# Kernel tuning notes

Measured on AMD Instinct MI355X. Metric: run time of the kernel, lower is better.

## Reference

```python
import jax, jax.numpy as jnp
import numpy as np

H, DK = 16, 64
D = H * DK  # d_model = 1024
B, S = 2, 2048


def setup_inputs() -> dict:
    key = jax.random.key(0)
    ks = jax.random.split(key, 11)
    std = 1.0 / np.sqrt(D)
    inp = {
        "query": jax.random.normal(ks[0], (B, S, D), dtype=jnp.float32),
        "key": jax.random.normal(ks[1], (B, S, D), dtype=jnp.float32),
        "value": jax.random.normal(ks[2], (B, S, D), dtype=jnp.float32),
        "Wq": jax.random.normal(ks[3], (D, D), dtype=jnp.float32) * std,
        "bq": jnp.zeros((D,), dtype=jnp.float32),
        "Wk": jax.random.normal(ks[4], (D, D), dtype=jnp.float32) * std,
        "bk": jnp.zeros((D,), dtype=jnp.float32),
        "Wv": jax.random.normal(ks[5], (D, D), dtype=jnp.float32) * std,
        "bv": jnp.zeros((D,), dtype=jnp.float32),
        "Wo": jax.random.normal(ks[6], (D, D), dtype=jnp.float32) * std,
        "bo": jnp.zeros((D,), dtype=jnp.float32),
    }
    return inp


def reference(query, key, value, Wq, bq, Wk, bk, Wv, bv, Wo, bo):
    # torch.nn.Linear convention: y = x @ W.T + b
    def split_heads(x):
        b, s, _ = x.shape
        return x.reshape(b, s, H, DK).transpose(0, 2, 1, 3)  # [B,H,S,DK]

    q = split_heads(query @ Wq.T + bq)
    k = split_heads(key @ Wk.T + bk)
    v = split_heads(value @ Wv.T + bv)

    scale = 1.0 / jnp.sqrt(jnp.asarray(DK, dtype=q.dtype))
    scores = jnp.einsum("bhqd,bhkd->bhqk", q, k) * scale  # [B,H,S,S]
    p_attn = jax.nn.softmax(scores, axis=-1)
    ctx = jnp.einsum("bhqk,bhkd->bhqd", p_attn, v)  # [B,H,S,DK]

    ctx = ctx.transpose(0, 2, 1, 3).reshape(query.shape[0], -1, H * DK)
    return ctx @ Wo.T + bo
```

## Files before the change

kernel.cpp:

```cpp
#include <hip/hip_runtime.h>
#include <stdint.h>

#define BATCH 2
#define SEQ   2048
#define NHEAD 16
#define DK    64
#define DMODEL 1024
#define MROWS (BATCH*SEQ)

typedef __attribute__((ext_vector_type(8))) __bf16 bf16x8;
typedef __attribute__((ext_vector_type(4))) float f32x4;
typedef __attribute__((ext_vector_type(8))) unsigned short u16x8;
typedef __attribute__((ext_vector_type(4))) unsigned short u16x4;

#define QSCALE 0.18033688f

__device__ __forceinline__ unsigned short f2bf(float f) {
  union { float f; uint32_t u; } c; c.f = f;
  uint32_t u = c.u;
  return (unsigned short)((u + 0x7fffu + ((u >> 16) & 1u)) >> 16);
}

__device__ __forceinline__ void gld16(const void* g, void* lds) {
  __builtin_amdgcn_global_load_lds(
      (const __attribute__((address_space(1))) void*)g,
      (__attribute__((address_space(3))) void*)lds,
      16, 0, 0);
}

__global__ __launch_bounds__(256)
void cvt_all(const float* __restrict__ q, const float* __restrict__ k, const float* __restrict__ v,
             const float* __restrict__ Wq, const float* __restrict__ Wk,
             const float* __restrict__ Wv, const float* __restrict__ Wo,
             unsigned short* __restrict__ Xq, unsigned short* __restrict__ Xk,
             unsigned short* __restrict__ Xv,
             unsigned short* __restrict__ Wqb, unsigned short* __restrict__ Wkb,
             unsigned short* __restrict__ Wvb, unsigned short* __restrict__ Wob) {
  int blk = blockIdx.x;
  const float* in; unsigned short* out; int base;
  if (blk < 6144) {
    int ti = blk >> 11;
    in  = (ti == 0) ? q  : (ti == 1) ? k  : v;
    out = (ti == 0) ? Xq : (ti == 1) ? Xk : Xv;
    base = (blk & 2047) * 2048;
  } else {
    int ti = (blk - 6144) >> 9;
    in  = (ti == 0) ? Wq  : (ti == 1) ? Wk  : (ti == 2) ? Wv  : Wo;
    out = (ti == 0) ? Wqb : (ti == 1) ? Wkb : (ti == 2) ? Wvb : Wob;
    base = ((blk - 6144) & 511) * 2048;
  }
  int i = base + threadIdx.x * 8;
  float4 a = *(const float4*)(in + i);
  float4 b = *(const float4*)(in + i + 4);
  u16x8 o;
  o[0]=f2bf(a.x); o[1]=f2bf(a.y); o[2]=f2bf(a.z); o[3]=f2bf(a.w);
  o[4]=f2bf(b.x); o[5]=f2bf(b.y); o[6]=f2bf(b.z); o[7]=f2bf(b.w);
  *(u16x8*)(out + i) = o;
}

template <int MODE>
__device__ __forceinline__ void gemm_body(unsigned short* __restrict__ lA,
                                          unsigned short* __restrict__ lB,
                                          const unsigned short* __restrict__ X,
                                          const unsigned short* __restrict__ W,
                                          const float* __restrict__ bias,
                                          unsigned short* __restrict__ Yb,
                                          float* __restrict__ Yf,
                                          int rowBase, int colBase) {
  const int t = threadIdx.x;
  const int lane = t & 63, wave = t >> 6;
  const int cl = lane & 15, qd = lane >> 4;
  const int wm = wave >> 1, wn = wave & 1;
  const int srow = t >> 3, sslot = t & 7;

  int aoff[2][4], boff[2][4];
  #pragma unroll
  for (int ks = 0; ks < 2; ks++)
    #pragma unroll
    for (int i = 0; i < 4; i++) {
      int ra = wm * 64 + i * 16 + cl;
      aoff[ks][i] = ra * 64 + ((ks * 4 + qd) ^ (ra & 7)) * 8;
      int rb = wn * 64 + i * 16 + cl;
      boff[ks][i] = rb * 64 + ((ks * 4 + qd) ^ (rb & 7)) * 8;
    }
  const unsigned short* xp[4];
  const unsigned short* wp[4];
  #pragma unroll
  for (int i = 0; i < 4; i++) {
    int r = i * 32 + srow;
    int chunk = sslot ^ (r & 7);
    xp[i] = X + (size_t)(rowBase + r) * DMODEL + chunk * 8;
    wp[i] = W + (size_t)(colBase + r) * DMODEL + chunk * 8;
  }

  f32x4 zero = {0.f, 0.f, 0.f, 0.f};
  f32x4 acc[4][4];
  for (int mt = 0; mt < 4; mt++) for (int nt = 0; nt < 4; nt++) acc[mt][nt] = zero;

  for (int k0 = 0; k0 < DMODEL; k0 += 64) {
    __syncthreads();
    #pragma unroll
    for (int i = 0; i < 4; i++) {
      gld16(xp[i], (char*)lA + i * 4096 + wave * 1024);
      gld16(wp[i], (char*)lB + i * 4096 + wave * 1024);
      xp[i] += 64; wp[i] += 64;
    }
    __syncthreads();
    #pragma unroll
    for (int ks = 0; ks < 2; ks++) {
      bf16x8 af[4], bfr[4];
      #pragma unroll
      for (int mt = 0; mt < 4; mt++) af[mt] = *(const bf16x8*)&lA[aoff[ks][mt]];
      #pragma unroll
      for (int nt = 0; nt < 4; nt++) bfr[nt] = *(const bf16x8*)&lB[boff[ks][nt]];
      #pragma unroll
      for (int mt = 0; mt < 4; mt++)
        #pragma unroll
        for (int nt = 0; nt < 4; nt++) {
          if (MODE == 2)
            acc[mt][nt] = __builtin_amdgcn_mfma_f32_16x16x32_bf16(af[mt], bfr[nt], acc[mt][nt], 0, 0, 0);
          else
            acc[mt][nt] = __builtin_amdgcn_mfma_f32_16x16x32_bf16(bfr[nt], af[mt], acc[mt][nt], 0, 0, 0);
        }
    }
  }

  if (MODE == 2) {
    #pragma unroll
    for (int mt = 0; mt < 4; mt++) {
      int row0 = rowBase + wm * 64 + mt * 16 + qd * 4;
      int bb = row0 >> 11;
      int s_in = row0 & 2047;
      int blk = s_in & ~63;
      int n4 = (s_in & 63) >> 2;
      int l4 = n4 & 7;
      int pos = 8 * (n4 >> 3) + ((l4 < 4) ? 2 * l4 : 2 * (l4 - 4) + 1);
      #pragma unroll
      for (int nt = 0; nt < 4; nt++) {
        int c = colBase + wn * 64 + nt * 16 + cl;
        float bv = bias[c];
        int hh = c >> 6, d = c & 63;
        u16x4 v;
        #pragma unroll
        for (int r = 0; r < 4; r++) v[r] = f2bf(acc[mt][nt][r] + bv);
        *(u16x4*)&Yb[(size_t)((bb * NHEAD + hh) * 64 + d) * SEQ + blk + pos * 4] = v;
      }
    }
  } else {
    #pragma unroll
    for (int nt = 0; nt < 4; nt++) {
      int col = colBase + wn * 64 + nt * 16 + qd * 4;
      f32x4 bv4 = *(const f32x4*)&bias[col];
      #pragma unroll
      for (int mt = 0; mt < 4; mt++) {
        int row = rowBase + wm * 64 + mt * 16 + cl;
        if (MODE == 3) {
          f32x4 v;
          #pragma unroll
          for (int r = 0; r < 4; r++) v[r] = acc[mt][nt][r] + bv4[r];
          *(f32x4*)&Yf[(size_t)row * DMODEL + col] = v;
        } else {
          u16x4 v;
          #pragma unroll
          for (int r = 0; r < 4; r++) {
            float x = acc[mt][nt][r] + bv4[r];
            v[r] = f2bf(MODE == 1 ? x * QSCALE : x);
          }
          *(u16x4*)&Yb[(size_t)row * DMODEL + col] = v;
        }
      }
    }
  }
}

__global__ __launch_bounds__(256)
void gemm_qkv(const unsigned short* __restrict__ Xq, const unsigned short* __restrict__ Xk,
              const unsigned short* __restrict__ Xv,
              const unsigned short* __restrict__ Wq, const unsigned short* __restrict__ Wk,
              const unsigned short* __restrict__ Wv,
              const float* __restrict__ bq, const float* __restrict__ bk,
              const float* __restrict__ bv,
              unsigned short* __restrict__ Q, unsigned short* __restrict__ K,
              unsigned short* __restrict__ VT) {
  __shared__ unsigned short lA[128 * 64];
  __shared__ unsigned short lB[128 * 64];
  int id = blockIdx.x;
  int by = id & 31, bx = id >> 5;
  int z = blockIdx.z;
  if (z == 0)      gemm_body<1>(lA, lB, Xq, Wq, bq, Q,  nullptr, by * 128, bx * 128);
  else if (z == 1) gemm_body<0>(lA, lB, Xk, Wk, bk, K,  nullptr, by * 128, bx * 128);
  else             gemm_body<2>(lA, lB, Xv, Wv, bv, VT, nullptr, by * 128, bx * 128);
}

__global__ __launch_bounds__(256)
void gemm_out(const unsigned short* __restrict__ CTX, const unsigned short* __restrict__ Wo,
              const float* __restrict__ bo, float* __restrict__ out) {
  __shared__ unsigned short lA[128 * 64];
  __shared__ unsigned short lB[128 * 64];
  int id = blockIdx.x;
  int by = id & 31, bx = id >> 5;
  gemm_body<3>(lA, lB, CTX, Wo, bo, nullptr, out, by * 128, bx * 128);
}

__global__ __launch_bounds__(256)
void attn(const unsigned short* __restrict__ Q, const unsigned short* __restrict__ K,
          const unsigned short* __restrict__ VT, unsigned short* __restrict__ CTX) {
  __shared__ unsigned short lK[2 * 64 * 64];
  __shared__ unsigned short lV[2 * 64 * 64];
  const int t = threadIdx.x, lane = t & 63, wave = t >> 6;
  const int cl = lane & 15, qd = lane >> 4;
  const int flat = blockIdx.x + 16 * blockIdx.y + 256 * blockIdx.z;
  const int loc = flat >> 3;
  const int p = (flat & 7) * 4 + (loc >> 4);
  const int qt = loc & 15, h = p & 15, b = p >> 4;
  const int srow = t >> 3, sslot = t & 7;

  #pragma unroll
  for (int half = 0; half < 2; half++)
    #pragma unroll
    for (int i = 0; i < 2; i++) {
      int r = i * 32 + srow;
      int chunk = sslot ^ (r & 7);
      gld16(Q + (size_t)(b * SEQ + qt * 128 + half * 64 + r) * DMODEL + h * 64 + chunk * 8,
            (char*)lK + half * 8192 + i * 4096 + wave * 1024);
    }
  __syncthreads();
  bf16x8 qf[2][2];
  #pragma unroll
  for (int qg = 0; qg < 2; qg++)
    #pragma unroll
    for (int ks = 0; ks < 2; ks++) {
      int r = wave * 16 + cl;
      int slot = (ks * 4 + qd) ^ (r & 7);
      qf[qg][ks] = *(const bf16x8*)&lK[qg * 4096 + r * 64 + slot * 8];
    }
  __syncthreads();

  int ka[8], va[8];
  #pragma unroll
  for (int ks = 0; ks < 2; ks++)
    #pragma unroll
    for (int nt = 0; nt < 4; nt++) {
      int rk = nt * 16 + cl;
      ka[ks * 4 + nt] = rk * 64 + ((ks * 4 + qd) ^ (rk & 7)) * 8;
    }
  #pragma unroll
  for (int ntp = 0; ntp < 2; ntp++)
    #pragma unroll
    for (int dt = 0; dt < 4; dt++) {
      int d = dt * 16 + cl;
      va[ntp * 4 + dt] = d * 64 + ((4 * ntp + qd) ^ (d & 7)) * 8;
    }

  const unsigned short* kp[2];
  const unsigned short* vp[2];
  #pragma unroll
  for (int i = 0; i < 2; i++) {
    int r = i * 32 + srow;
    int chunk = sslot ^ (r & 7);
    kp[i] = K + (size_t)(b * SEQ + r) * DMODEL + h * 64 + chunk * 8;
    vp[i] = VT + (size_t)((b * NHEAD + h) * 64 + r) * SEQ + chunk * 8;
    gld16(kp[i], (char*)lK + i * 4096 + wave * 1024);
    gld16(vp[i], (char*)lV + i * 4096 + wave * 1024);
    kp[i] += 64 * DMODEL; vp[i] += 64;
  }

  f32x4 zero = {0.f, 0.f, 0.f, 0.f};
  f32x4 o[2][4];
  f32x4 osum[2];
  #pragma unroll
  for (int qg = 0; qg < 2; qg++) {
    #pragma unroll
    for (int dt = 0; dt < 4; dt++) o[qg][dt] = zero;
    osum[qg] = zero;
  }
  bf16x8 ones;
  #pragma unroll
  for (int j = 0; j < 8; j++) ones[j] = (__bf16)1.0f;

  #pragma unroll 2
  for (int kt = 0; kt < SEQ / 64; kt++) {
    const int cb = (kt & 1) * 4096;
    __syncthreads();
    if (kt + 1 < SEQ / 64) {
      const int nb = ((kt + 1) & 1) * 8192;
      #pragma unroll
      for (int i = 0; i < 2; i++) {
        gld16(kp[i], (char*)lK + nb + i * 4096 + wave * 1024);
        gld16(vp[i], (char*)lV + nb + i * 4096 + wave * 1024);
        kp[i] += 64 * DMODEL; vp[i] += 64;
      }
    }

    f32x4 sc[2][4];
    #pragma unroll
    for (int qg = 0; qg < 2; qg++)
      #pragma unroll
      for (int nt = 0; nt < 4; nt++) sc[qg][nt] = zero;
    #pragma unroll
    for (int ks = 0; ks < 2; ks++)
      #pragma unroll
      for (int nt = 0; nt < 4; nt++) {
        bf16x8 kf = *(const bf16x8*)&lK[cb + ka[ks * 4 + nt]];
        sc[0][nt] = __builtin_amdgcn_mfma_f32_16x16x32_bf16(kf, qf[0][ks], sc[0][nt], 0, 0, 0);
        sc[1][nt] = __builtin_amdgcn_mfma_f32_16x16x32_bf16(kf, qf[1][ks], sc[1][nt], 0, 0, 0);
      }

    bf16x8 pb[2][2];
    #pragma unroll
    for (int qg = 0; qg < 2; qg++)
      #pragma unroll
      for (int ntp = 0; ntp < 2; ntp++) {
        bf16x8 x;
        #pragma unroll
        for (int j = 0; j < 4; j++)
          x[j] = (__bf16)__builtin_amdgcn_exp2f(sc[qg][2 * ntp][j]);
        #pragma unroll
        for (int j = 0; j < 4; j++)
          x[4 + j] = (__bf16)__builtin_amdgcn_exp2f(sc[qg][2 * ntp + 1][j]);
        pb[qg][ntp] = x;
      }

    #pragma unroll
    for (int qg = 0; qg < 2; qg++) {
      osum[qg] = __builtin_amdgcn_mfma_f32_16x16x32_bf16(ones, pb[qg][0], osum[qg], 0, 0, 0);
      osum[qg] = __builtin_amdgcn_mfma_f32_16x16x32_bf16(ones, pb[qg][1], osum[qg], 0, 0, 0);
    }

    #pragma unroll
    for (int ntp = 0; ntp < 2; ntp++)
      #pragma unroll
      for (int dt = 0; dt < 4; dt++) {
        bf16x8 vf = *(const bf16x8*)&lV[cb + va[ntp * 4 + dt]];
        o[0][dt] = __builtin_amdgcn_mfma_f32_16x16x32_bf16(vf, pb[0][ntp], o[0][dt], 0, 0, 0);
        o[1][dt] = __builtin_amdgcn_mfma_f32_16x16x32_bf16(vf, pb[1][ntp], o[1][dt], 0, 0, 0);
      }
  }

  #pragma unroll
  for (int qg = 0; qg < 2; qg++) {
    float inv = 1.f / osum[qg][0];
    int row = b * SEQ + qt * 128 + qg * 64 + wave * 16 + cl;
    #pragma unroll
    for (int dt = 0; dt < 4; dt++) {
      u16x4 v;
      #pragma unroll
      for (int r = 0; r < 4; r++) v[r] = f2bf(o[qg][dt][r] * inv);
      *(u16x4*)&CTX[(size_t)row * DMODEL + h * 64 + dt * 16 + qd * 4] = v;
    }
  }
}

extern "C" void kernel_launch(void* const* d_in, const int* in_sizes, int n_in,
                              void* d_out, int out_size, void* d_ws, size_t ws_size,
                              hipStream_t stream) {
  const float* q  = (const float*)d_in[0];
  const float* k  = (const float*)d_in[1];
  const float* v  = (const float*)d_in[2];
  const float* Wq = (const float*)d_in[3]; const float* bq = (const float*)d_in[4];
  const float* Wk = (const float*)d_in[5]; const float* bk = (const float*)d_in[6];
  const float* Wv = (const float*)d_in[7]; const float* bv = (const float*)d_in[8];
  const float* Wo = (const float*)d_in[9]; const float* bo = (const float*)d_in[10];
  float* out = (float*)d_out;

  char* ws = (char*)d_ws;
  const size_t MB = 1u << 20;
  unsigned short* Xq  = (unsigned short*)(ws + 0 * MB);
  unsigned short* Xk  = (unsigned short*)(ws + 8 * MB);
  unsigned short* Xv  = (unsigned short*)(ws + 16 * MB);
  unsigned short* Wqb = (unsigned short*)(ws + 24 * MB);
  unsigned short* Wkb = (unsigned short*)(ws + 26 * MB);
  unsigned short* Wvb = (unsigned short*)(ws + 28 * MB);
  unsigned short* Wob = (unsigned short*)(ws + 70 * MB);
  unsigned short* Qp  = (unsigned short*)(ws + 32 * MB);
  unsigned short* Kp  = (unsigned short*)(ws + 40 * MB);
  unsigned short* VT  = (unsigned short*)(ws + 48 * MB);
  unsigned short* CTX = (unsigned short*)(ws + 56 * MB);

  cvt_all<<<8192, 256, 0, stream>>>(q, k, v, Wq, Wk, Wv, Wo,
                                    Xq, Xk, Xv, Wqb, Wkb, Wvb, Wob);

  gemm_qkv<<<dim3(256, 1, 3), 256, 0, stream>>>(
      Xq, Xk, Xv, Wqb, Wkb, Wvb, bq, bk, bv, Qp, Kp, VT);

  attn<<<dim3(SEQ / 128, NHEAD, BATCH), 256, 0, stream>>>(Qp, Kp, VT, CTX);

  gemm_out<<<256, 256, 0, stream>>>(CTX, Wob, bo, out);
}
```

Measured before the change: 218.9 us.

## Split-K the output projection with atomic adds and bias-initialized output

The output projection GEMM is split into two K halves, doubling the grid from 256 to 512 blocks so more of the GPU's compute units are occupied. Each half adds its partial result into the fp32 output with per-element atomic adds. The output is first filled with the bias by extra blocks in the conversion kernel. This adds an extra full pass writing the output, plus atomic traffic, and makes the fp32 summation order nondeterministic.

```diff
diff --git a/kernel.cpp b/kernel.cpp
--- a/kernel.cpp
+++ b/kernel.cpp
@@ -32,11 +32,20 @@
 void cvt_all(const float* __restrict__ q, const float* __restrict__ k, const float* __restrict__ v,
              const float* __restrict__ Wq, const float* __restrict__ Wk,
              const float* __restrict__ Wv, const float* __restrict__ Wo,
+             const float* __restrict__ bo, float* __restrict__ outp,
              unsigned short* __restrict__ Xq, unsigned short* __restrict__ Xk,
              unsigned short* __restrict__ Xv,
              unsigned short* __restrict__ Wqb, unsigned short* __restrict__ Wkb,
              unsigned short* __restrict__ Wvb, unsigned short* __restrict__ Wob) {
   int blk = blockIdx.x;
+  if (blk >= 8192) {
+    int i = (blk - 8192) * 2048 + threadIdx.x * 8;
+    float4 b0 = *(const float4*)&bo[i & (DMODEL - 1)];
+    float4 b1 = *(const float4*)&bo[(i + 4) & (DMODEL - 1)];
+    *(float4*)&outp[i] = b0;
+    *(float4*)&outp[i + 4] = b1;
+    return;
+  }
   const float* in; unsigned short* out; int base;
   if (blk < 6144) {
     int ti = blk >> 11;
@@ -66,7 +75,7 @@
                                           const float* __restrict__ bias,
                                           unsigned short* __restrict__ Yb,
                                           float* __restrict__ Yf,
-                                          int rowBase, int colBase) {
+                                          int rowBase, int colBase, int kb, int ke) {
   const int t = threadIdx.x;
   const int lane = t & 63, wave = t >> 6;
   const int cl = lane & 15, qd = lane >> 4;
@@ -89,15 +98,15 @@
   for (int i = 0; i < 4; i++) {
     int r = i * 32 + srow;
     int chunk = sslot ^ (r & 7);
-    xp[i] = X + (size_t)(rowBase + r) * DMODEL + chunk * 8;
-    wp[i] = W + (size_t)(colBase + r) * DMODEL + chunk * 8;
+    xp[i] = X + (size_t)(rowBase + r) * DMODEL + kb + chunk * 8;
+    wp[i] = W + (size_t)(colBase + r) * DMODEL + kb + chunk * 8;
   }
 
   f32x4 zero = {0.f, 0.f, 0.f, 0.f};
   f32x4 acc[4][4];
   for (int mt = 0; mt < 4; mt++) for (int nt = 0; nt < 4; nt++) acc[mt][nt] = zero;
 
-  for (int k0 = 0; k0 < DMODEL; k0 += 64) {
+  for (int k0 = kb; k0 < ke; k0 += 64) {
     __syncthreads();
     #pragma unroll
     for (int i = 0; i < 4; i++) {
@@ -150,11 +159,15 @@
     #pragma unroll
     for (int nt = 0; nt < 4; nt++) {
       int col = colBase + wn * 64 + nt * 16 + qd * 4;
-      f32x4 bv4 = *(const f32x4*)&bias[col];
+      f32x4 bv4 = (MODE == 4) ? zero : *(const f32x4*)&bias[col];
       #pragma unroll
       for (int mt = 0; mt < 4; mt++) {
         int row = rowBase + wm * 64 + mt * 16 + cl;
-        if (MODE == 3) {
+        if (MODE == 4) {
+          #pragma unroll
+          for (int r = 0; r < 4; r++)
+            unsafeAtomicAdd(&Yf[(size_t)row * DMODEL + col + r], acc[mt][nt][r]);
+        } else if (MODE == 3) {
           f32x4 v;
           #pragma unroll
           for (int r = 0; r < 4; r++) v[r] = acc[mt][nt][r] + bv4[r];
@@ -187,19 +200,21 @@
   int id = blockIdx.x;
   int by = id & 31, bx = id >> 5;
   int z = blockIdx.z;
-  if (z == 0)      gemm_body<1>(lA, lB, Xq, Wq, bq, Q,  nullptr, by * 128, bx * 128);
-  else if (z == 1) gemm_body<0>(lA, lB, Xk, Wk, bk, K,  nullptr, by * 128, bx * 128);
-  else             gemm_body<2>(lA, lB, Xv, Wv, bv, VT, nullptr, by * 128, bx * 128);
+  if (z == 0)      gemm_body<1>(lA, lB, Xq, Wq, bq, Q,  nullptr, by * 128, bx * 128, 0, DMODEL);
+  else if (z == 1) gemm_body<0>(lA, lB, Xk, Wk, bk, K,  nullptr, by * 128, bx * 128, 0, DMODEL);
+  else             gemm_body<2>(lA, lB, Xv, Wv, bv, VT, nullptr, by * 128, bx * 128, 0, DMODEL);
 }
 
 __global__ __launch_bounds__(256)
 void gemm_out(const unsigned short* __restrict__ CTX, const unsigned short* __restrict__ Wo,
-              const float* __restrict__ bo, float* __restrict__ out) {
+              float* __restrict__ out) {
   __shared__ unsigned short lA[128 * 64];
   __shared__ unsigned short lB[128 * 64];
   int id = blockIdx.x;
-  int by = id & 31, bx = id >> 5;
-  gemm_body<3>(lA, lB, CTX, Wo, bo, nullptr, out, by * 128, bx * 128);
+  int sp = id & 1;
+  int by = (id >> 1) & 31, bx = id >> 6;
+  gemm_body<4>(lA, lB, CTX, Wo, nullptr, nullptr, out,
+               by * 128, bx * 128, sp * 512, sp * 512 + 512);
 }
 
 __global__ __launch_bounds__(256)
@@ -377,13 +392,13 @@
   unsigned short* VT  = (unsigned short*)(ws + 48 * MB);
   unsigned short* CTX = (unsigned short*)(ws + 56 * MB);
 
-  cvt_all<<<8192, 256, 0, stream>>>(q, k, v, Wq, Wk, Wv, Wo,
-                                    Xq, Xk, Xv, Wqb, Wkb, Wvb, Wob);
+  cvt_all<<<10240, 256, 0, stream>>>(q, k, v, Wq, Wk, Wv, Wo, bo, out,
+                                     Xq, Xk, Xv, Wqb, Wkb, Wvb, Wob);
 
   gemm_qkv<<<dim3(256, 1, 3), 256, 0, stream>>>(
       Xq, Xk, Xv, Wqb, Wkb, Wvb, bq, bk, bv, Qp, Kp, VT);
 
   attn<<<dim3(SEQ / 128, NHEAD, BATCH), 256, 0, stream>>>(Qp, Kp, VT, CTX);
 
-  gemm_out<<<256, 256, 0, stream>>>(CTX, Wob, bo, out);
-}
+  gemm_out<<<512, 256, 0, stream>>>(CTX, Wob, out);
+}
```

New measurement: 310.9 us. 1.42x slower.
